# Performance work log

Hardware: AMD Instinct MI355X
Metric: run time of the kernel (lower is better)

The kernel has to match this reference:

```python
import jax, jax.numpy as jnp
import numpy as np

NHEAD = 8
K_NEIGH = 16


def setup_inputs() -> dict:
    key = jax.random.key(0)
    ks = jax.random.split(key, 6)
    B, L, D = 4, 4096, 512
    x = jax.random.normal(ks[0], (B, L, D), dtype=jnp.float32)
    positions = jax.random.uniform(ks[1], (B, L, 3), dtype=jnp.float32)
    in_proj_w = jax.random.normal(ks[2], (3 * D, D), dtype=jnp.float32) * 0.02
    in_proj_b = jax.random.normal(ks[3], (3 * D,), dtype=jnp.float32) * 0.02
    out_proj_w = jax.random.normal(ks[4], (D, D), dtype=jnp.float32) * 0.02
    out_proj_b = jax.random.normal(ks[5], (D,), dtype=jnp.float32) * 0.02
    return {"x": x, "positions": positions, "in_proj_w": in_proj_w,
            "in_proj_b": in_proj_b, "out_proj_w": out_proj_w, "out_proj_b": out_proj_b}


def _sparse_attention(x, positions, in_proj_w, in_proj_b, out_proj_w, out_proj_b):
    B, L, D = x.shape
    H, dh = NHEAD, D // NHEAD
    K = min(K_NEIGH, L)
    scale = 1.0 / jnp.sqrt(jnp.asarray(dh, x.dtype))

    # Pairwise distances [B, L, L]; topk smallest -> neighbor indices [B, L, K].
    diff = positions[:, :, None, :] - positions[:, None, :, :]
    dist = jnp.sqrt(jnp.sum(diff * diff, axis=-1))
    _, nbr = jax.lax.top_k(-dist, K)  # [B, L, K]

    Wq, Wk, Wv = in_proj_w[:D], in_proj_w[D:2 * D], in_proj_w[2 * D:]
    bq, bk, bv = in_proj_b[:D], in_proj_b[D:2 * D], in_proj_b[2 * D:]

    # Query is x[b, i] itself (self is always its own nearest neighbor at dist 0),
    # so the selected attention row equals attention with query x[b, i] over neighbors.
    q = ((x @ Wq.T + bq) * scale).reshape(B, L, H, dh)

    # Gather neighbor features: [B, L, K, D]
    b_idx = jnp.arange(B)[:, None, None]
    local_x = x[b_idx, nbr]
    k = (local_x @ Wk.T + bk).reshape(B, L, K, H, dh)
    v = (local_x @ Wv.T + bv).reshape(B, L, K, H, dh)

    scores = jnp.einsum('blhd,blkhd->blhk', q, k)
    attn = jax.nn.softmax(scores, axis=-1)
    ctx = jnp.einsum('blhk,blkhd->blhd', attn, v).reshape(B, L, D)
    out = ctx @ out_proj_w.T + out_proj_b

    # Faithful fallback: if i not among its neighbors, pass through x[b, i].
    is_in = jnp.any(nbr == jnp.arange(L)[None, :, None], axis=-1)  # [B, L]
    return jnp.where(is_in[..., None], out, x)


def reference(x, positions, in_proj_w, in_proj_b, out_proj_w, out_proj_b):
    return _sparse_attention(x, positions, in_proj_w, in_proj_b, out_proj_w, out_proj_b)
```

## Files before the change

kernel.cpp:

```cpp
#include <hip/hip_runtime.h>
#include <cfloat>
#include <cmath>

constexpr int B = 4;
constexpr int L = 4096;
constexpr int D = 512;
constexpr int NH = 8;
constexpr int DH = 64;
constexpr int KN = 16;
constexpr int M = B * L;
constexpr int N_IN = 3 * D;
constexpr int NCELL = 512;

typedef __attribute__((ext_vector_type(8))) short short8;
typedef __attribute__((ext_vector_type(4))) float f32x4;
typedef unsigned short ushort;

__device__ __forceinline__ ushort f2bf(float f) {
  unsigned u = __float_as_uint(f);
  u = u + 0x7fffu + ((u >> 16) & 1u);
  return (ushort)(u >> 16);
}
__device__ __forceinline__ float bf2f(ushort h) {
  return __uint_as_float(((unsigned)h) << 16);
}
__device__ __forceinline__ float dot8(const uint4 qu, const uint4 ku, float a) {
  a = fmaf(bf2f((ushort)qu.x), bf2f((ushort)ku.x), a);
  a = fmaf(bf2f((ushort)(qu.x >> 16)), bf2f((ushort)(ku.x >> 16)), a);
  a = fmaf(bf2f((ushort)qu.y), bf2f((ushort)ku.y), a);
  a = fmaf(bf2f((ushort)(qu.y >> 16)), bf2f((ushort)(ku.y >> 16)), a);
  a = fmaf(bf2f((ushort)qu.z), bf2f((ushort)ku.z), a);
  a = fmaf(bf2f((ushort)(qu.z >> 16)), bf2f((ushort)(ku.z >> 16)), a);
  a = fmaf(bf2f((ushort)qu.w), bf2f((ushort)ku.w), a);
  a = fmaf(bf2f((ushort)(qu.w >> 16)), bf2f((ushort)(ku.w >> 16)), a);
  return a;
}
__device__ __forceinline__ void acc8(float wgt, const uint4 vv, float (&acc)[8]) {
  acc[0] = fmaf(wgt, bf2f((ushort)vv.x), acc[0]);
  acc[1] = fmaf(wgt, bf2f((ushort)(vv.x >> 16)), acc[1]);
  acc[2] = fmaf(wgt, bf2f((ushort)vv.y), acc[2]);
  acc[3] = fmaf(wgt, bf2f((ushort)(vv.y >> 16)), acc[3]);
  acc[4] = fmaf(wgt, bf2f((ushort)vv.z), acc[4]);
  acc[5] = fmaf(wgt, bf2f((ushort)(vv.z >> 16)), acc[5]);
  acc[6] = fmaf(wgt, bf2f((ushort)vv.w), acc[6]);
  acc[7] = fmaf(wgt, bf2f((ushort)(vv.w >> 16)), acc[7]);
}
__device__ __forceinline__ uint2 pack4hi(const float4 v) {
  uint2 o;
  o.x = (unsigned)f2bf(v.x) | ((unsigned)f2bf(v.y) << 16);
  o.y = (unsigned)f2bf(v.z) | ((unsigned)f2bf(v.w) << 16);
  return o;
}
__device__ __forceinline__ void gload16(const void* g, void* l) {
  __builtin_amdgcn_global_load_lds(
      (const __attribute__((address_space(1))) void*)g,
      (__attribute__((address_space(3))) void*)l, 16, 0, 0);
}
__device__ __forceinline__ int morton3(int x, int y, int z) {
  int m = 0;
#pragma unroll
  for (int i = 0; i < 3; ++i)
    m |= (((x >> i) & 1) << (3 * i + 2)) | (((y >> i) & 1) << (3 * i + 1)) |
         (((z >> i) & 1) << (3 * i));
  return m;
}

constexpr int TP = 65;
constexpr int TOPK_BLKS = B * (L / 8);
constexpr int SORT_BLKS = B;
constexpr int CVTX_BLKS = 1024;
constexpr int CVTW_BLKS = 256;
constexpr int STAGE0_BLKS = TOPK_BLKS + SORT_BLKS + CVTX_BLKS + CVTW_BLKS;

__global__ __launch_bounds__(512) void stage0_kernel(
    const float* __restrict__ pos, const float* __restrict__ x,
    const float* __restrict__ in_w, const float* __restrict__ out_w,
    int* __restrict__ nbr, int* __restrict__ isin, int* __restrict__ qorder,
    ushort* __restrict__ xb, ushort* __restrict__ iwh,
    ushort* __restrict__ owh, ushort* __restrict__ owl) {
  __shared__ float sxT[64 * TP], syT[64 * TP], szT[64 * TP];
  __shared__ unsigned long long lst[8 * 64];
  __shared__ int hist[NCELL];
  __shared__ int scanbuf[NCELL];

  const int bid = blockIdx.x;
  const int tid = threadIdx.x;

  if (bid < TOPK_BLKS) {
    const int wave = tid >> 6;
    const int lane = tid & 63;
    const int b = bid >> 9;
    const int l = (bid & 511) * 8 + wave;
    const int row = b * L + l;

    const float* p = pos + (size_t)b * L * 3;
    for (int i = tid; i < L; i += 512) {
      const int a = (i & 63) * TP + (i >> 6);
      sxT[a] = p[3 * i + 0];
      syT[a] = p[3 * i + 1];
      szT[a] = p[3 * i + 2];
    }
    __syncthreads();

    const int qa = (l & 63) * TP + (l >> 6);
    const float qx = sxT[qa], qy = syT[qa], qz = szT[qa];

    float mA = FLT_MAX, mB2 = FLT_MAX, mC = FLT_MAX, mD2 = FLT_MAX;
    const int base = lane * TP;
    for (int j = 0; j < 64; j += 4) {
#define D2(t, acc)                                                   \
      {                                                              \
        const int a = base + j + t;                                  \
        const float dx = qx - sxT[a], dy = qy - syT[a], dz = qz - szT[a]; \
        acc = fminf(acc, fmaf(dx, dx, fmaf(dy, dy, dz * dz)));       \
      }
      D2(0, mA) D2(1, mB2) D2(2, mC) D2(3, mD2)
#undef D2
    }
    const unsigned mbits = __float_as_uint(fminf(fminf(mA, mB2), fminf(mC, mD2)));

    unsigned lo = 1, hi = 0x40400001u;
    while (lo < hi) {
      const unsigned mid = (lo + hi) >> 1;
      const int c = __popcll(__ballot(mbits < mid));
      if (c >= 16) hi = mid; else lo = mid + 1;
    }
    const unsigned P = lo + 16;

    int cnt = 0;
    unsigned long long am = __ballot(mbits < P);
    const unsigned long long below = (1ull << lane) - 1ull;
    while (am) {
      const int pl = (int)__builtin_ctzll(am);
      am &= am - 1;
      const int a = pl * TP + lane;
      const float dx = qx - sxT[a], dy = qy - syT[a], dz = qz - szT[a];
      const float d2 = fmaf(dx, dx, fmaf(dy, dy, dz * dz));
      const bool hit = __float_as_uint(d2) < P;
      const unsigned long long msk = __ballot(hit);
      if (hit) {
        const int slot = cnt + __popcll(msk & below);
        if (slot < 64) {
          const unsigned c = (unsigned)(lane * 64 + pl);
          lst[wave * 64 + slot] =
              ((unsigned long long)__float_as_uint(sqrtf(d2)) << 32) | c;
        }
      }
      cnt += __popcll(msk);
    }
    const int n = min(cnt, 64);

    const unsigned long long mine = (lane < n) ? lst[wave * 64 + lane] : ~0ull;
    int r = 0;
    for (int i = 0; i < n; ++i) r += (lst[wave * 64 + i] < mine) ? 1 : 0;

    const int idx = (int)(unsigned)(mine & 0xffffffffu);
    const bool wr = (lane < n) && (r < 16);
    if (wr) nbr[(size_t)row * KN + r] = idx;
    const unsigned long long hit2 = __ballot(wr && idx == l);
    if (lane == 0) isin[row] = hit2 ? 1 : 0;

  } else if (bid < TOPK_BLKS + SORT_BLKS) {
    const int b = bid - TOPK_BLKS;
    const int t = tid;
    hist[t] = 0;
    __syncthreads();

    int cells[8], ranks[8];
    const float* p = pos + (size_t)b * L * 3;
#pragma unroll
    for (int q = 0; q < 8; ++q) {
      const int i = q * 512 + t;
      const int ix = min(7, max(0, (int)(p[3 * i + 0] * 8.f)));
      const int iy = min(7, max(0, (int)(p[3 * i + 1] * 8.f)));
      const int iz = min(7, max(0, (int)(p[3 * i + 2] * 8.f)));
      cells[q] = morton3(ix, iy, iz);
      ranks[q] = atomicAdd(&hist[cells[q]], 1);
    }
    __syncthreads();

    int accv = hist[t];
    const int orig = accv;
    scanbuf[t] = accv;
    __syncthreads();
    for (int s = 1; s < NCELL; s <<= 1) {
      const int o = (t >= s) ? scanbuf[t - s] : 0;
      __syncthreads();
      accv += o;
      scanbuf[t] = accv;
      __syncthreads();
    }
    hist[t] = accv - orig;
    __syncthreads();

#pragma unroll
    for (int q = 0; q < 8; ++q) {
      const int i = q * 512 + t;
      qorder[b * L + hist[cells[q]] + ranks[q]] = i;
    }

  } else if (bid < TOPK_BLKS + SORT_BLKS + CVTX_BLKS) {
    const int vb = bid - TOPK_BLKS - SORT_BLKS;
    const int n8 = M * D / 8;
    for (int i = vb * 512 + tid; i < n8; i += CVTX_BLKS * 512) {
      const float4 v0 = reinterpret_cast<const float4*>(x)[i * 2];
      const float4 v1 = reinterpret_cast<const float4*>(x)[i * 2 + 1];
      uint4 o;
      const uint2 a = pack4hi(v0), b2 = pack4hi(v1);
      o.x = a.x; o.y = a.y; o.z = b2.x; o.w = b2.y;
      reinterpret_cast<uint4*>(xb)[i] = o;
    }

  } else {
    const int vb = bid - TOPK_BLKS - SORT_BLKS - CVTX_BLKS;
    const int ni8 = N_IN * D / 8;
    const int no8 = D * D / 8;
    for (int i = vb * 512 + tid; i < ni8 + no8; i += CVTW_BLKS * 512) {
      if (i < ni8) {
        const float4 v0 = reinterpret_cast<const float4*>(in_w)[i * 2];
        const float4 v1 = reinterpret_cast<const float4*>(in_w)[i * 2 + 1];
        uint4 o;
        const uint2 a = pack4hi(v0), b2 = pack4hi(v1);
        o.x = a.x; o.y = a.y; o.z = b2.x; o.w = b2.y;
        reinterpret_cast<uint4*>(iwh)[i] = o;
      } else {
        const int j = i - ni8;
        const float4 v0 = reinterpret_cast<const float4*>(out_w)[j * 2];
        const float4 v1 = reinterpret_cast<const float4*>(out_w)[j * 2 + 1];
        uint4 oh, ol;
        const uint2 a = pack4hi(v0), b2 = pack4hi(v1);
        oh.x = a.x; oh.y = a.y; oh.z = b2.x; oh.w = b2.y;
        const float4 r0 = make_float4(v0.x - bf2f(f2bf(v0.x)), v0.y - bf2f(f2bf(v0.y)),
                                      v0.z - bf2f(f2bf(v0.z)), v0.w - bf2f(f2bf(v0.w)));
        const float4 r1 = make_float4(v1.x - bf2f(f2bf(v1.x)), v1.y - bf2f(f2bf(v1.y)),
                                      v1.z - bf2f(f2bf(v1.z)), v1.w - bf2f(f2bf(v1.w)));
        const uint2 c = pack4hi(r0), d2 = pack4hi(r1);
        ol.x = c.x; ol.y = c.y; ol.z = d2.x; ol.w = d2.y;
        reinterpret_cast<uint4*>(owh)[j] = oh;
        reinterpret_cast<uint4*>(owl)[j] = ol;
      }
    }
  }
}

constexpr int BM = 128, BN = 128;
constexpr int BK2 = 64;

__global__ __launch_bounds__(256) void gemm_in(const ushort* __restrict__ A,
                                               const ushort* __restrict__ W,
                                               const float* __restrict__ bias,
                                               ushort* __restrict__ qb,
                                               ushort* __restrict__ kb,
                                               ushort* __restrict__ vb) {
  __shared__ ushort Ah[BM * BK2];
  __shared__ ushort Bh[BN * BK2];

  const int tid = threadIdx.x;
  const int m0 = blockIdx.x * BM;
  const int n0 = blockIdx.y * BN;

  const int wv = tid >> 6;
  const int lane = tid & 63;
  const int srow0 = wv * 8 + (lane >> 3);
  const int gchunk = (lane & 7) ^ (lane >> 3);
  const ushort* Asrc = A + (size_t)(m0 + srow0) * D + gchunk * 8;
  const ushort* Wsrc = W + (size_t)(n0 + srow0) * D + gchunk * 8;
  ushort* AhB0 = Ah + (wv * 8) * BK2;
  ushort* AhB1 = Ah + (wv * 8 + 32) * BK2;
  ushort* AhB2 = Ah + (wv * 8 + 64) * BK2;
  ushort* AhB3 = Ah + (wv * 8 + 96) * BK2;
  ushort* BhB0 = Bh + (wv * 8) * BK2;
  ushort* BhB1 = Bh + (wv * 8 + 32) * BK2;
  ushort* BhB2 = Bh + (wv * 8 + 64) * BK2;
  ushort* BhB3 = Bh + (wv * 8 + 96) * BK2;

  const int wr0 = (wv >> 1) * 64;
  const int wc0 = (wv & 1) * 64;
  const int fr_row = lane & 15;
  const int cbase = lane >> 4;
  const int rx = lane & 7;

  f32x4 acc[4][4];
#pragma unroll
  for (int i = 0; i < 4; ++i)
#pragma unroll
    for (int j = 0; j < 4; ++j) acc[i][j] = {0.f, 0.f, 0.f, 0.f};

  for (int k0 = 0; k0 < D; k0 += BK2) {
    __syncthreads();
    gload16(Asrc + k0, AhB0);
    gload16(Asrc + (size_t)32 * D + k0, AhB1);
    gload16(Asrc + (size_t)64 * D + k0, AhB2);
    gload16(Asrc + (size_t)96 * D + k0, AhB3);
    gload16(Wsrc + k0, BhB0);
    gload16(Wsrc + (size_t)32 * D + k0, BhB1);
    gload16(Wsrc + (size_t)64 * D + k0, BhB2);
    gload16(Wsrc + (size_t)96 * D + k0, BhB3);
    __syncthreads();

#pragma unroll
    for (int kk = 0; kk < 2; ++kk) {
      const int slot = (kk * 4 + cbase) ^ rx;
      short8 ah[4];
#pragma unroll
      for (int fr = 0; fr < 4; ++fr)
        ah[fr] = *reinterpret_cast<const short8*>(
            &Ah[(wr0 + fr * 16 + fr_row) * BK2 + slot * 8]);
#pragma unroll
      for (int fc = 0; fc < 4; ++fc) {
        const short8 bh = *reinterpret_cast<const short8*>(
            &Bh[(wc0 + fc * 16 + fr_row) * BK2 + slot * 8]);
#pragma unroll
        for (int fr = 0; fr < 4; ++fr)
          acc[fr][fc] = __builtin_amdgcn_mfma_f32_16x16x32_bf16(ah[fr], bh, acc[fr][fc], 0, 0, 0);
      }
    }
  }

  const int region = n0 >> 9;
  ushort* outb = region == 0 ? qb : (region == 1 ? kb : vb);
  const float scl = region == 0 ? 0.125f : 1.0f;
  const int nloc0 = (n0 & 511) + wc0;
#pragma unroll
  for (int fr = 0; fr < 4; ++fr) {
#pragma unroll
    for (int r = 0; r < 4; ++r) {
      const int grow = m0 + wr0 + fr * 16 + (lane >> 4) * 4 + r;
#pragma unroll
      for (int fc = 0; fc < 4; ++fc) {
        const int cc = fc * 16 + (lane & 15);
        const float v = (acc[fr][fc][r] + bias[n0 + wc0 + cc]) * scl;
        outb[(size_t)grow * D + nloc0 + cc] = f2bf(v);
      }
    }
  }
}

__global__ __launch_bounds__(256) void gemm_out(const ushort* __restrict__ A,
                                                const ushort* __restrict__ Wh,
                                                const ushort* __restrict__ Wl,
                                                const float* __restrict__ bias,
                                                float* __restrict__ C,
                                                const float* __restrict__ X,
                                                const int* __restrict__ isin) {
  __shared__ ushort Ah[BM * BK2];
  __shared__ ushort Bh[BN * BK2];
  __shared__ ushort Bl[BN * BK2];

  const int tid = threadIdx.x;
  const int m0 = blockIdx.x * BM;
  const int n0 = blockIdx.y * BN;

  const int wv = tid >> 6;
  const int lane = tid & 63;
  const int srow0 = wv * 8 + (lane >> 3);
  const int gchunk = (lane & 7) ^ (lane >> 3);
  const ushort* Asrc = A + (size_t)(m0 + srow0) * D + gchunk * 8;
  const ushort* Hsrc = Wh + (size_t)(n0 + srow0) * D + gchunk * 8;
  const ushort* Lsrc = Wl + (size_t)(n0 + srow0) * D + gchunk * 8;
  ushort* AhB0 = Ah + (wv * 8) * BK2;
  ushort* AhB1 = Ah + (wv * 8 + 32) * BK2;
  ushort* AhB2 = Ah + (wv * 8 + 64) * BK2;
  ushort* AhB3 = Ah + (wv * 8 + 96) * BK2;
  ushort* BhB0 = Bh + (wv * 8) * BK2;
  ushort* BhB1 = Bh + (wv * 8 + 32) * BK2;
  ushort* BhB2 = Bh + (wv * 8 + 64) * BK2;
  ushort* BhB3 = Bh + (wv * 8 + 96) * BK2;
  ushort* BlB0 = Bl + (wv * 8) * BK2;
  ushort* BlB1 = Bl + (wv * 8 + 32) * BK2;
  ushort* BlB2 = Bl + (wv * 8 + 64) * BK2;
  ushort* BlB3 = Bl + (wv * 8 + 96) * BK2;

  const int wr0 = (wv >> 1) * 64;
  const int wc0 = (wv & 1) * 64;
  const int fr_row = lane & 15;
  const int cbase = lane >> 4;
  const int rx = lane & 7;

  f32x4 acc[4][4];
#pragma unroll
  for (int i = 0; i < 4; ++i)
#pragma unroll
    for (int j = 0; j < 4; ++j) acc[i][j] = {0.f, 0.f, 0.f, 0.f};

  for (int k0 = 0; k0 < D; k0 += BK2) {
    __syncthreads();
    gload16(Asrc + k0, AhB0);
    gload16(Asrc + (size_t)32 * D + k0, AhB1);
    gload16(Asrc + (size_t)64 * D + k0, AhB2);
    gload16(Asrc + (size_t)96 * D + k0, AhB3);
    gload16(Hsrc + k0, BhB0);
    gload16(Hsrc + (size_t)32 * D + k0, BhB1);
    gload16(Hsrc + (size_t)64 * D + k0, BhB2);
    gload16(Hsrc + (size_t)96 * D + k0, BhB3);
    gload16(Lsrc + k0, BlB0);
    gload16(Lsrc + (size_t)32 * D + k0, BlB1);
    gload16(Lsrc + (size_t)64 * D + k0, BlB2);
    gload16(Lsrc + (size_t)96 * D + k0, BlB3);
    __syncthreads();

#pragma unroll
    for (int kk = 0; kk < 2; ++kk) {
      const int slot = (kk * 4 + cbase) ^ rx;
      short8 ah[4];
#pragma unroll
      for (int fr = 0; fr < 4; ++fr)
        ah[fr] = *reinterpret_cast<const short8*>(
            &Ah[(wr0 + fr * 16 + fr_row) * BK2 + slot * 8]);
#pragma unroll
      for (int fc = 0; fc < 4; ++fc) {
        const short8 bh = *reinterpret_cast<const short8*>(
            &Bh[(wc0 + fc * 16 + fr_row) * BK2 + slot * 8]);
        const short8 bl = *reinterpret_cast<const short8*>(
            &Bl[(wc0 + fc * 16 + fr_row) * BK2 + slot * 8]);
#pragma unroll
        for (int fr = 0; fr < 4; ++fr) {
          acc[fr][fc] = __builtin_amdgcn_mfma_f32_16x16x32_bf16(ah[fr], bh, acc[fr][fc], 0, 0, 0);
          acc[fr][fc] = __builtin_amdgcn_mfma_f32_16x16x32_bf16(ah[fr], bl, acc[fr][fc], 0, 0, 0);
        }
      }
    }
  }

#pragma unroll
  for (int fr = 0; fr < 4; ++fr) {
#pragma unroll
    for (int r = 0; r < 4; ++r) {
      const int grow = m0 + wr0 + fr * 16 + (lane >> 4) * 4 + r;
      const int ok = isin[grow];
#pragma unroll
      for (int fc = 0; fc < 4; ++fc) {
        const int gcol = n0 + wc0 + fc * 16 + (lane & 15);
        float v = acc[fr][fc][r] + bias[gcol];
        if (!ok) v = X[(size_t)grow * D + gcol];
        C[(size_t)grow * D + gcol] = v;
      }
    }
  }
}

__global__ __launch_bounds__(256) void attn_kernel(const ushort* __restrict__ qb,
                                                   const ushort* __restrict__ kb,
                                                   const ushort* __restrict__ vb,
                                                   const int* __restrict__ nbr,
                                                   const int* __restrict__ qorder,
                                                   ushort* __restrict__ ctx) {
  const int wave = threadIdx.x >> 6;
  const int lane = threadIdx.x & 63;
  const int xcd = blockIdx.x & 7;
  const int chunk = blockIdx.x >> 3;
  const int b = xcd >> 1;
  const int slot = ((xcd & 1) * 512 + chunk) * 4 + wave;
  const int l = qorder[b * L + slot];
  const int bl = b * L + l;
  const int bbase = b * L;
  const int* nb = nbr + (size_t)bl * KN;

  const int h = lane >> 3;
  const int n0 = lane & 7;
  const int glane = h * 8;

  const ushort* qp = qb + (size_t)bl * D + h * DH;
  uint4 qv[8];
#pragma unroll
  for (int i = 0; i < 8; ++i)
    qv[i] = *reinterpret_cast<const uint4*>(qp + i * 8);

  const int j0 = nb[n0];
  const int j1 = nb[n0 + 8];
  float a0 = 0.f, a1 = 0.f;
  {
    const ushort* kr0 = kb + (size_t)(bbase + j0) * D + h * DH;
    const ushort* kr1 = kb + (size_t)(bbase + j1) * D + h * DH;
#pragma unroll
    for (int i = 0; i < 8; ++i) {
      a0 = dot8(qv[i], *reinterpret_cast<const uint4*>(kr0 + i * 8), a0);
      a1 = dot8(qv[i], *reinterpret_cast<const uint4*>(kr1 + i * 8), a1);
    }
  }

  float mx = fmaxf(a0, a1);
  mx = fmaxf(mx, __shfl_xor(mx, 1));
  mx = fmaxf(mx, __shfl_xor(mx, 2));
  mx = fmaxf(mx, __shfl_xor(mx, 4));
  const float e0 = expf(a0 - mx), e1 = expf(a1 - mx);
  float sm = e0 + e1;
  sm += __shfl_xor(sm, 1);
  sm += __shfl_xor(sm, 2);
  sm += __shfl_xor(sm, 4);
  const float inv = 1.0f / sm;
  const float w0 = e0 * inv, w1 = e1 * inv;

  float ww[KN];
  int jj[KN];
#pragma unroll
  for (int n = 0; n < KN; ++n) {
    const int src = glane + (n & 7);
    ww[n] = __shfl((n < 8) ? w0 : w1, src);
    jj[n] = __shfl((n < 8) ? j0 : j1, src);
  }

  const int d0 = n0 * 8;
  const ushort* vbase = vb + (size_t)bbase * D + h * DH + d0;
  float acc[8];
#pragma unroll
  for (int i = 0; i < 8; ++i) acc[i] = 0.f;

#pragma unroll
  for (int g = 0; g < KN; g += 4) {
    const uint4 va0 = *reinterpret_cast<const uint4*>(vbase + (size_t)jj[g] * D);
    const uint4 va1 = *reinterpret_cast<const uint4*>(vbase + (size_t)jj[g + 1] * D);
    const uint4 va2 = *reinterpret_cast<const uint4*>(vbase + (size_t)jj[g + 2] * D);
    const uint4 va3 = *reinterpret_cast<const uint4*>(vbase + (size_t)jj[g + 3] * D);
    acc8(ww[g], va0, acc);
    acc8(ww[g + 1], va1, acc);
    acc8(ww[g + 2], va2, acc);
    acc8(ww[g + 3], va3, acc);
  }

  uint4 o;
  o.x = (unsigned)f2bf(acc[0]) | ((unsigned)f2bf(acc[1]) << 16);
  o.y = (unsigned)f2bf(acc[2]) | ((unsigned)f2bf(acc[3]) << 16);
  o.z = (unsigned)f2bf(acc[4]) | ((unsigned)f2bf(acc[5]) << 16);
  o.w = (unsigned)f2bf(acc[6]) | ((unsigned)f2bf(acc[7]) << 16);
  *reinterpret_cast<uint4*>(ctx + (size_t)bl * D + h * DH + d0) = o;
}

extern "C" void kernel_launch(void* const* d_in, const int* in_sizes, int n_in,
                              void* d_out, int out_size, void* d_ws, size_t ws_size,
                              hipStream_t stream) {
  const float* x     = (const float*)d_in[0];
  const float* pos   = (const float*)d_in[1];
  const float* in_w  = (const float*)d_in[2];
  const float* in_b  = (const float*)d_in[3];
  const float* out_w = (const float*)d_in[4];
  const float* out_b = (const float*)d_in[5];
  float* out = (float*)d_out;

  const size_t nbr_bytes  = (size_t)M * KN * sizeof(int);
  const size_t isin_bytes = (size_t)M * sizeof(int);
  const size_t half_bytes = (size_t)M * D * sizeof(ushort);
  const size_t iwh_bytes  = (size_t)N_IN * D * sizeof(ushort);
  const size_t ow_bytes   = (size_t)D * D * sizeof(ushort);
  const size_t sort_bytes = (size_t)M * sizeof(int);
  const size_t need = nbr_bytes + isin_bytes + 5 * half_bytes +
                      iwh_bytes + 2 * ow_bytes + sort_bytes + 16384;
  if (ws_size < need) return;

  char* w = (char*)d_ws;
  int*    nbr    = (int*)w;    w += (nbr_bytes + 255) & ~(size_t)255;
  int*    isin   = (int*)w;    w += (isin_bytes + 255) & ~(size_t)255;
  ushort* xb     = (ushort*)w; w += (half_bytes + 255) & ~(size_t)255;
  ushort* qb     = (ushort*)w; w += (half_bytes + 255) & ~(size_t)255;
  ushort* kb     = (ushort*)w; w += (half_bytes + 255) & ~(size_t)255;
  ushort* vb     = (ushort*)w; w += (half_bytes + 255) & ~(size_t)255;
  ushort* ctxb   = (ushort*)w; w += (half_bytes + 255) & ~(size_t)255;
  ushort* iwh    = (ushort*)w; w += (iwh_bytes + 255) & ~(size_t)255;
  ushort* owh    = (ushort*)w; w += (ow_bytes + 255) & ~(size_t)255;
  ushort* owl    = (ushort*)w; w += (ow_bytes + 255) & ~(size_t)255;
  int*    qorder = (int*)w;

  stage0_kernel<<<STAGE0_BLKS, 512, 0, stream>>>(
      pos, x, in_w, out_w, nbr, isin, qorder, xb, iwh, owh, owl);

  gemm_in<<<dim3(M / BM, N_IN / BN), 256, 0, stream>>>(xb, iwh, in_b, qb, kb, vb);

  attn_kernel<<<M / 4, 256, 0, stream>>>(qb, kb, vb, nbr, qorder, ctxb);

  gemm_out<<<dim3(M / BM, D / BN), 256, 0, stream>>>(ctxb, owh, owl, out_b, out, x, isin);
}
```

Measured before the change: 150.5 us.

## Fuse neighbor top-k search into the attention kernel, dropping the nbr buffer

Moves the per-query nearest-neighbor search out of stage0 and into the attention kernel. Neighbor indices now stay in shared memory and feed the K/V gathers directly, so the global nbr array and its write/read round trip are gone. Stage0 becomes lighter and no longer serializes the top-k work ahead of the GEMM. The trade-off is that each attention block must reload all positions into LDS (about 50KB), which lowers occupancy for the attention phase, and the top-k search now runs after the input GEMM instead of beside it.

Measured after the change: 151.6 us. Within noise of the previous version (+0.7%).

```diff
diff --git a/kernel.cpp b/kernel.cpp
--- a/kernel.cpp
+++ b/kernel.cpp
@@ -65,103 +65,25 @@
   return m;
 }
 
-constexpr int TP = 65;
-constexpr int TOPK_BLKS = B * (L / 8);
 constexpr int SORT_BLKS = B;
 constexpr int CVTX_BLKS = 1024;
 constexpr int CVTW_BLKS = 256;
-constexpr int STAGE0_BLKS = TOPK_BLKS + SORT_BLKS + CVTX_BLKS + CVTW_BLKS;
+constexpr int STAGE0_BLKS = SORT_BLKS + CVTX_BLKS + CVTW_BLKS;
 
 __global__ __launch_bounds__(512) void stage0_kernel(
     const float* __restrict__ pos, const float* __restrict__ x,
     const float* __restrict__ in_w, const float* __restrict__ out_w,
-    int* __restrict__ nbr, int* __restrict__ isin, int* __restrict__ qorder,
-    ushort* __restrict__ xb, ushort* __restrict__ iwh,
-    ushort* __restrict__ owh, ushort* __restrict__ owl) {
-  __shared__ float sxT[64 * TP], syT[64 * TP], szT[64 * TP];
-  __shared__ unsigned long long lst[8 * 64];
+    int* __restrict__ qorder, ushort* __restrict__ xb,
+    ushort* __restrict__ iwh, ushort* __restrict__ owh,
+    ushort* __restrict__ owl) {
   __shared__ int hist[NCELL];
   __shared__ int scanbuf[NCELL];
 
   const int bid = blockIdx.x;
   const int tid = threadIdx.x;
 
-  if (bid < TOPK_BLKS) {
-    const int wave = tid >> 6;
-    const int lane = tid & 63;
-    const int b = bid >> 9;
-    const int l = (bid & 511) * 8 + wave;
-    const int row = b * L + l;
-
-    const float* p = pos + (size_t)b * L * 3;
-    for (int i = tid; i < L; i += 512) {
-      const int a = (i & 63) * TP + (i >> 6);
-      sxT[a] = p[3 * i + 0];
-      syT[a] = p[3 * i + 1];
-      szT[a] = p[3 * i + 2];
-    }
-    __syncthreads();
-
-    const int qa = (l & 63) * TP + (l >> 6);
-    const float qx = sxT[qa], qy = syT[qa], qz = szT[qa];
-
-    float mA = FLT_MAX, mB2 = FLT_MAX, mC = FLT_MAX, mD2 = FLT_MAX;
-    const int base = lane * TP;
-    for (int j = 0; j < 64; j += 4) {
-#define D2(t, acc)                                                   \
-      {                                                              \
-        const int a = base + j + t;                                  \
-        const float dx = qx - sxT[a], dy = qy - syT[a], dz = qz - szT[a]; \
-        acc = fminf(acc, fmaf(dx, dx, fmaf(dy, dy, dz * dz)));       \
-      }
-      D2(0, mA) D2(1, mB2) D2(2, mC) D2(3, mD2)
-#undef D2
-    }
-    const unsigned mbits = __float_as_uint(fminf(fminf(mA, mB2), fminf(mC, mD2)));
-
-    unsigned lo = 1, hi = 0x40400001u;
-    while (lo < hi) {
-      const unsigned mid = (lo + hi) >> 1;
-      const int c = __popcll(__ballot(mbits < mid));
-      if (c >= 16) hi = mid; else lo = mid + 1;
-    }
-    const unsigned P = lo + 16;
-
-    int cnt = 0;
-    unsigned long long am = __ballot(mbits < P);
-    const unsigned long long below = (1ull << lane) - 1ull;
-    while (am) {
-      const int pl = (int)__builtin_ctzll(am);
-      am &= am - 1;
-      const int a = pl * TP + lane;
-      const float dx = qx - sxT[a], dy = qy - syT[a], dz = qz - szT[a];
-      const float d2 = fmaf(dx, dx, fmaf(dy, dy, dz * dz));
-      const bool hit = __float_as_uint(d2) < P;
-      const unsigned long long msk = __ballot(hit);
-      if (hit) {
-        const int slot = cnt + __popcll(msk & below);
-        if (slot < 64) {
-          const unsigned c = (unsigned)(lane * 64 + pl);
-          lst[wave * 64 + slot] =
-              ((unsigned long long)__float_as_uint(sqrtf(d2)) << 32) | c;
-        }
-      }
-      cnt += __popcll(msk);
-    }
-    const int n = min(cnt, 64);
-
-    const unsigned long long mine = (lane < n) ? lst[wave * 64 + lane] : ~0ull;
-    int r = 0;
-    for (int i = 0; i < n; ++i) r += (lst[wave * 64 + i] < mine) ? 1 : 0;
-
-    const int idx = (int)(unsigned)(mine & 0xffffffffu);
-    const bool wr = (lane < n) && (r < 16);
-    if (wr) nbr[(size_t)row * KN + r] = idx;
-    const unsigned long long hit2 = __ballot(wr && idx == l);
-    if (lane == 0) isin[row] = hit2 ? 1 : 0;
-
-  } else if (bid < TOPK_BLKS + SORT_BLKS) {
-    const int b = bid - TOPK_BLKS;
+  if (bid < SORT_BLKS) {
+    const int b = bid;
     const int t = tid;
     hist[t] = 0;
     __syncthreads();
@@ -199,8 +121,8 @@
       qorder[b * L + hist[cells[q]] + ranks[q]] = i;
     }
 
-  } else if (bid < TOPK_BLKS + SORT_BLKS + CVTX_BLKS) {
-    const int vb = bid - TOPK_BLKS - SORT_BLKS;
+  } else if (bid < SORT_BLKS + CVTX_BLKS) {
+    const int vb = bid - SORT_BLKS;
     const int n8 = M * D / 8;
     for (int i = vb * 512 + tid; i < n8; i += CVTX_BLKS * 512) {
       const float4 v0 = reinterpret_cast<const float4*>(x)[i * 2];
@@ -212,7 +134,7 @@
     }
 
   } else {
-    const int vb = bid - TOPK_BLKS - SORT_BLKS - CVTX_BLKS;
+    const int vb = bid - SORT_BLKS - CVTX_BLKS;
     const int ni8 = N_IN * D / 8;
     const int no8 = D * D / 8;
     for (int i = vb * 512 + tid; i < ni8 + no8; i += CVTW_BLKS * 512) {
@@ -243,6 +165,163 @@
   }
 }
 
+constexpr int TP = 65;
+
+__global__ __launch_bounds__(512) void topk_attn_kernel(
+    const float* __restrict__ pos, const ushort* __restrict__ qb,
+    const ushort* __restrict__ kb, const ushort* __restrict__ vb,
+    const int* __restrict__ qorder, int* __restrict__ isin,
+    ushort* __restrict__ ctx) {
+  __shared__ float sxT[64 * TP], syT[64 * TP], szT[64 * TP];
+  __shared__ unsigned long long lst[8 * 64];
+  __shared__ int nbw[8][KN];
+
+  const int wave = threadIdx.x >> 6;
+  const int lane = threadIdx.x & 63;
+  const int xcd = blockIdx.x & 7;
+  const int chunk = blockIdx.x >> 3;
+  const int b = xcd >> 1;
+  const int slot = ((xcd & 1) * 256 + chunk) * 8 + wave;
+  const int l = qorder[b * L + slot];
+  const int row = b * L + l;
+  const int bbase = b * L;
+
+  const float* p = pos + (size_t)b * L * 3;
+  for (int i = threadIdx.x; i < L; i += 512) {
+    const int a = (i & 63) * TP + (i >> 6);
+    sxT[a] = p[3 * i + 0];
+    syT[a] = p[3 * i + 1];
+    szT[a] = p[3 * i + 2];
+  }
+  __syncthreads();
+
+  const int qa = (l & 63) * TP + (l >> 6);
+  const float qx = sxT[qa], qy = syT[qa], qz = szT[qa];
+
+  float mA = FLT_MAX, mB2 = FLT_MAX, mC = FLT_MAX, mD2 = FLT_MAX;
+  const int base = lane * TP;
+  for (int j = 0; j < 64; j += 4) {
+#define D2(t, acc)                                                   \
+    {                                                                \
+      const int a = base + j + t;                                    \
+      const float dx = qx - sxT[a], dy = qy - syT[a], dz = qz - szT[a]; \
+      acc = fminf(acc, fmaf(dx, dx, fmaf(dy, dy, dz * dz)));         \
+    }
+    D2(0, mA) D2(1, mB2) D2(2, mC) D2(3, mD2)
+#undef D2
+  }
+  const unsigned mbits = __float_as_uint(fminf(fminf(mA, mB2), fminf(mC, mD2)));
+
+  unsigned lo = 1, hi = 0x40400001u;
+  while (lo < hi) {
+    const unsigned mid = (lo + hi) >> 1;
+    const int c = __popcll(__ballot(mbits < mid));
+    if (c >= 16) hi = mid; else lo = mid + 1;
+  }
+  const unsigned P = lo + 16;
+
+  int cnt = 0;
+  unsigned long long am = __ballot(mbits < P);
+  const unsigned long long below = (1ull << lane) - 1ull;
+  while (am) {
+    const int pl = (int)__builtin_ctzll(am);
+    am &= am - 1;
+    const int a = pl * TP + lane;
+    const float dx = qx - sxT[a], dy = qy - syT[a], dz = qz - szT[a];
+    const float d2 = fmaf(dx, dx, fmaf(dy, dy, dz * dz));
+    const bool hit = __float_as_uint(d2) < P;
+    const unsigned long long msk = __ballot(hit);
+    if (hit) {
+      const int slot2 = cnt + __popcll(msk & below);
+      if (slot2 < 64) {
+        const unsigned c = (unsigned)(lane * 64 + pl);
+        lst[wave * 64 + slot2] =
+            ((unsigned long long)__float_as_uint(sqrtf(d2)) << 32) | c;
+      }
+    }
+    cnt += __popcll(msk);
+  }
+  const int n = min(cnt, 64);
+
+  const unsigned long long mine = (lane < n) ? lst[wave * 64 + lane] : ~0ull;
+  int r = 0;
+  for (int i = 0; i < n; ++i) r += (lst[wave * 64 + i] < mine) ? 1 : 0;
+
+  const int nidx = (int)(unsigned)(mine & 0xffffffffu);
+  const bool wr = (lane < n) && (r < 16);
+  if (wr) nbw[wave][r] = nidx;
+  const unsigned long long hit2 = __ballot(wr && nidx == l);
+  if (lane == 0) isin[row] = hit2 ? 1 : 0;
+
+  const int h = lane >> 3;
+  const int n0 = lane & 7;
+  const int glane = h * 8;
+
+  const ushort* qp = qb + (size_t)row * D + h * DH;
+  uint4 qv[8];
+#pragma unroll
+  for (int i = 0; i < 8; ++i)
+    qv[i] = *reinterpret_cast<const uint4*>(qp + i * 8);
+
+  const int j0 = nbw[wave][n0];
+  const int j1 = nbw[wave][n0 + 8];
+  float a0 = 0.f, a1 = 0.f;
+  {
+    const ushort* kr0 = kb + (size_t)(bbase + j0) * D + h * DH;
+    const ushort* kr1 = kb + (size_t)(bbase + j1) * D + h * DH;
+#pragma unroll
+    for (int i = 0; i < 8; ++i) {
+      a0 = dot8(qv[i], *reinterpret_cast<const uint4*>(kr0 + i * 8), a0);
+      a1 = dot8(qv[i], *reinterpret_cast<const uint4*>(kr1 + i * 8), a1);
+    }
+  }
+
+  float mx = fmaxf(a0, a1);
+  mx = fmaxf(mx, __shfl_xor(mx, 1));
+  mx = fmaxf(mx, __shfl_xor(mx, 2));
+  mx = fmaxf(mx, __shfl_xor(mx, 4));
+  const float e0 = expf(a0 - mx), e1 = expf(a1 - mx);
+  float sm = e0 + e1;
+  sm += __shfl_xor(sm, 1);
+  sm += __shfl_xor(sm, 2);
+  sm += __shfl_xor(sm, 4);
+  const float inv = 1.0f / sm;
+  const float w0 = e0 * inv, w1 = e1 * inv;
+
+  float ww[KN];
+  int jj[KN];
+#pragma unroll
+  for (int nn = 0; nn < KN; ++nn) {
+    ww[nn] = __shfl((nn < 8) ? w0 : w1, glane + (nn & 7));
+    jj[nn] = nbw[wave][nn];
+  }
+
+  const int d0 = n0 * 8;
+  const ushort* vbase = vb + (size_t)bbase * D + h * DH + d0;
+  float acc[8];
+#pragma unroll
+  for (int i = 0; i < 8; ++i) acc[i] = 0.f;
+
+#pragma unroll
+  for (int g = 0; g < KN; g += 4) {
+    const uint4 va0 = *reinterpret_cast<const uint4*>(vbase + (size_t)jj[g] * D);
+    const uint4 va1 = *reinterpret_cast<const uint4*>(vbase + (size_t)jj[g + 1] * D);
+    const uint4 va2 = *reinterpret_cast<const uint4*>(vbase + (size_t)jj[g + 2] * D);
+    const uint4 va3 = *reinterpret_cast<const uint4*>(vbase + (size_t)jj[g + 3] * D);
+    acc8(ww[g], va0, acc);
+    acc8(ww[g + 1], va1, acc);
+    acc8(ww[g + 2], va2, acc);
+    acc8(ww[g + 3], va3, acc);
+  }
+
+  uint4 o;
+  o.x = (unsigned)f2bf(acc[0]) | ((unsigned)f2bf(acc[1]) << 16);
+  o.y = (unsigned)f2bf(acc[2]) | ((unsigned)f2bf(acc[3]) << 16);
+  o.z = (unsigned)f2bf(acc[4]) | ((unsigned)f2bf(acc[5]) << 16);
+  o.w = (unsigned)f2bf(acc[6]) | ((unsigned)f2bf(acc[7]) << 16);
+  *reinterpret_cast<uint4*>(ctx + (size_t)row * D + h * DH + d0) = o;
+}
+
 constexpr int BM = 128, BN = 128;
 constexpr int BK2 = 64;
 
@@ -439,93 +518,6 @@
   }
 }
 
-__global__ __launch_bounds__(256) void attn_kernel(const ushort* __restrict__ qb,
-                                                   const ushort* __restrict__ kb,
-                                                   const ushort* __restrict__ vb,
-                                                   const int* __restrict__ nbr,
-                                                   const int* __restrict__ qorder,
-                                                   ushort* __restrict__ ctx) {
-  const int wave = threadIdx.x >> 6;
-  const int lane = threadIdx.x & 63;
-  const int xcd = blockIdx.x & 7;
-  const int chunk = blockIdx.x >> 3;
-  const int b = xcd >> 1;
-  const int slot = ((xcd & 1) * 512 + chunk) * 4 + wave;
-  const int l = qorder[b * L + slot];
-  const int bl = b * L + l;
-  const int bbase = b * L;
-  const int* nb = nbr + (size_t)bl * KN;
-
-  const int h = lane >> 3;
-  const int n0 = lane & 7;
-  const int glane = h * 8;
-
-  const ushort* qp = qb + (size_t)bl * D + h * DH;
-  uint4 qv[8];
-#pragma unroll
-  for (int i = 0; i < 8; ++i)
-    qv[i] = *reinterpret_cast<const uint4*>(qp + i * 8);
-
-  const int j0 = nb[n0];
-  const int j1 = nb[n0 + 8];
-  float a0 = 0.f, a1 = 0.f;
-  {
-    const ushort* kr0 = kb + (size_t)(bbase + j0) * D + h * DH;
-    const ushort* kr1 = kb + (size_t)(bbase + j1) * D + h * DH;
-#pragma unroll
-    for (int i = 0; i < 8; ++i) {
-      a0 = dot8(qv[i], *reinterpret_cast<const uint4*>(kr0 + i * 8), a0);
-      a1 = dot8(qv[i], *reinterpret_cast<const uint4*>(kr1 + i * 8), a1);
-    }
-  }
-
-  float mx = fmaxf(a0, a1);
-  mx = fmaxf(mx, __shfl_xor(mx, 1));
-  mx = fmaxf(mx, __shfl_xor(mx, 2));
-  mx = fmaxf(mx, __shfl_xor(mx, 4));
-  const float e0 = expf(a0 - mx), e1 = expf(a1 - mx);
-  float sm = e0 + e1;
-  sm += __shfl_xor(sm, 1);
-  sm += __shfl_xor(sm, 2);
-  sm += __shfl_xor(sm, 4);
-  const float inv = 1.0f / sm;
-  const float w0 = e0 * inv, w1 = e1 * inv;
-
-  float ww[KN];
-  int jj[KN];
-#pragma unroll
-  for (int n = 0; n < KN; ++n) {
-    const int src = glane + (n & 7);
-    ww[n] = __shfl((n < 8) ? w0 : w1, src);
-    jj[n] = __shfl((n < 8) ? j0 : j1, src);
-  }
-
-  const int d0 = n0 * 8;
-  const ushort* vbase = vb + (size_t)bbase * D + h * DH + d0;
-  float acc[8];
-#pragma unroll
-  for (int i = 0; i < 8; ++i) acc[i] = 0.f;
-
-#pragma unroll
-  for (int g = 0; g < KN; g += 4) {
-    const uint4 va0 = *reinterpret_cast<const uint4*>(vbase + (size_t)jj[g] * D);
-    const uint4 va1 = *reinterpret_cast<const uint4*>(vbase + (size_t)jj[g + 1] * D);
-    const uint4 va2 = *reinterpret_cast<const uint4*>(vbase + (size_t)jj[g + 2] * D);
-    const uint4 va3 = *reinterpret_cast<const uint4*>(vbase + (size_t)jj[g + 3] * D);
-    acc8(ww[g], va0, acc);
-    acc8(ww[g + 1], va1, acc);
-    acc8(ww[g + 2], va2, acc);
-    acc8(ww[g + 3], va3, acc);
-  }
-
-  uint4 o;
-  o.x = (unsigned)f2bf(acc[0]) | ((unsigned)f2bf(acc[1]) << 16);
-  o.y = (unsigned)f2bf(acc[2]) | ((unsigned)f2bf(acc[3]) << 16);
-  o.z = (unsigned)f2bf(acc[4]) | ((unsigned)f2bf(acc[5]) << 16);
-  o.w = (unsigned)f2bf(acc[6]) | ((unsigned)f2bf(acc[7]) << 16);
-  *reinterpret_cast<uint4*>(ctx + (size_t)bl * D + h * DH + d0) = o;
-}
-
 extern "C" void kernel_launch(void* const* d_in, const int* in_sizes, int n_in,
                               void* d_out, int out_size, void* d_ws, size_t ws_size,
                               hipStream_t stream) {
@@ -537,18 +529,16 @@
   const float* out_b = (const float*)d_in[5];
   float* out = (float*)d_out;
 
-  const size_t nbr_bytes  = (size_t)M * KN * sizeof(int);
   const size_t isin_bytes = (size_t)M * sizeof(int);
   const size_t half_bytes = (size_t)M * D * sizeof(ushort);
   const size_t iwh_bytes  = (size_t)N_IN * D * sizeof(ushort);
   const size_t ow_bytes   = (size_t)D * D * sizeof(ushort);
   const size_t sort_bytes = (size_t)M * sizeof(int);
-  const size_t need = nbr_bytes + isin_bytes + 5 * half_bytes +
+  const size_t need = isin_bytes + 5 * half_bytes +
                       iwh_bytes + 2 * ow_bytes + sort_bytes + 16384;
   if (ws_size < need) return;
 
   char* w = (char*)d_ws;
-  int*    nbr    = (int*)w;    w += (nbr_bytes + 255) & ~(size_t)255;
   int*    isin   = (int*)w;    w += (isin_bytes + 255) & ~(size_t)255;
   ushort* xb     = (ushort*)w; w += (half_bytes + 255) & ~(size_t)255;
   ushort* qb     = (ushort*)w; w += (half_bytes + 255) & ~(size_t)255;
@@ -561,11 +551,11 @@
   int*    qorder = (int*)w;
 
   stage0_kernel<<<STAGE0_BLKS, 512, 0, stream>>>(
-      pos, x, in_w, out_w, nbr, isin, qorder, xb, iwh, owh, owl);
+      pos, x, in_w, out_w, qorder, xb, iwh, owh, owl);
 
   gemm_in<<<dim3(M / BM, N_IN / BN), 256, 0, stream>>>(xb, iwh, in_b, qb, kb, vb);
 
-  attn_kernel<<<M / 4, 256, 0, stream>>>(qb, kb, vb, nbr, qorder, ctxb);
+  topk_attn_kernel<<<M / 8, 512, 0, stream>>>(pos, qb, kb, vb, qorder, isin, ctxb);
 
   gemm_out<<<dim3(M / BM, D / BN), 256, 0, stream>>>(ctxb, owh, owl, out_b, out, x, isin);
 }
```
